# Kernel optimization log

Measured on AMD Instinct MI355X. Metric: run time of the kernel, lower is better.

## Reference

```python
import jax, jax.numpy as jnp
import numpy as np
from jax.scipy.special import gammaln

B, N, K = 16, 65536, 64


def setup_inputs() -> dict:
    key = jax.random.key(0)
    k1, k2, k3, k4, k5 = jax.random.split(key, 5)
    x = jax.random.normal(k1, (B, N), dtype=jnp.float32)
    loc = jnp.full((1,), 0.5, dtype=jnp.float32)          # mean of Normal alpha prior
    scale = jnp.full((1,), -2.0, dtype=jnp.float32)       # softplus(-2) ~ 0.127
    epsilon = jax.random.normal(k3, (1,), dtype=jnp.float32)
    lags = jax.random.randint(k4, (K,), 1, N - 1, dtype=jnp.int64)
    return {"x": x, "loc": loc, "scale": scale, "epsilon": epsilon, "lags": lags}


def _stochastic_frac_deriv(x, alpha, lags):
    """Monte-Carlo Marchaud fractional derivative with k sampled memory lags.

    D^a f(t) ~ a/Gamma(1-a) * (N-1)/k * sum_m (f(t) - f(t - j_m)) * j_m^{-a-1}
    with the term masked out when t < j_m (history does not exist).
    """
    n = x.shape[-1]
    k = lags.shape[0]
    j = jnp.clip(lags, 1, n - 1)                      # [k]
    t = jnp.arange(n)                                 # [N]
    idx = jnp.maximum(t[None, :] - j[:, None], 0)     # [k, N]
    mask = (t[None, :] >= j[:, None]).astype(x.dtype) # [k, N]
    w = j.astype(x.dtype) ** (-(alpha + 1.0))         # kernel weight s^{-a-1}, [k]
    c = alpha * jnp.exp(-gammaln(1.0 - alpha)) * (n - 1) / k  # normalization * MC volume
    xg = x[:, idx]                                    # [B, k, N] gathered history
    contrib = (x[:, None, :] - xg) * (mask * w[:, None])[None, :, :]
    return c * contrib.sum(axis=1)                    # [B, N]


def reference(x, loc, scale, epsilon, lags):
    # reparameterized alpha ~ Normal(loc, softplus(scale))
    alpha = (loc + jax.nn.softplus(scale) * epsilon)[0]
    alpha = jnp.clip(alpha, 0.01, 0.99)               # keep fractional order valid
    return _stochastic_frac_deriv(x, alpha, lags)
```

## Files before the change

kernel.cpp:

```cpp
#include <hip/hip_runtime.h>

#define BB 16
#define NN 65536
#define KK 64
#define TPB 256
#define CHUNK 512
#define NBLK ((BB * NN) / CHUNK)

__device__ __forceinline__ float readlane_f(float v, int lane) {
    return __uint_as_float((unsigned)__builtin_amdgcn_readlane((int)__float_as_uint(v), lane));
}

__global__ __launch_bounds__(TPB, 4) void frac_deriv_kernel(
    const float* __restrict__ x,
    const float* __restrict__ loc,
    const float* __restrict__ scale,
    const float* __restrict__ eps,
    const int* __restrict__ lags,
    float* __restrict__ out)
{
    __shared__ int   js_raw[KK];
    __shared__ float ws_raw[KK];
    __shared__ int   js[KK];
    __shared__ float ws[KK];

    const int tid  = threadIdx.x;
    const int lane = tid & 63;

    const int bid = blockIdx.x;
    const int swz = (bid & 7) * (NBLK / 8) + (bid >> 3);
    const int b   = swz >> 7;
    const int q   = 127 - (swz & 127);
    const int T   = q * CHUNK;

    const float* __restrict__ xr = x + (size_t)b * NN;
    const float xt0 = xr[T + tid];
    const float xt1 = xr[T + 256 + tid];

    if (tid < KK) {
        double s  = (double)scale[0];
        double sp = (s > 20.0) ? s : log1p(exp(s));
        double a  = (double)loc[0] + sp * (double)eps[0];
        a = fmin(fmax(a, 0.01), 0.99);
        double c = a * exp(-lgamma(1.0 - a)) * ((double)(NN - 1) / (double)KK);
        int j = lags[tid];
        j = (j < 1) ? 1 : ((j > NN - 1) ? NN - 1 : j);
        js_raw[tid] = j;
        ws_raw[tid] = (float)(c * exp(-(a + 1.0) * log((double)j)));
    }
    __syncthreads();
    if (tid < KK) {
        const int j = js_raw[tid];
        int rank = 0;
        for (int k = 0; k < KK; ++k) {
            const int jk = js_raw[k];
            rank += (int)((jk < j) || (jk == j && k < tid));
        }
        js[rank] = j;
        ws[rank] = ws_raw[tid];
    }
    __syncthreads();

    const int   jv = js[lane];
    const float wv = ws[lane];
    const int cf = __popcll(__ballot(jv <= T));
    const int cp = __popcll(__ballot(jv <= T + (CHUNK - 1)));
    const int cf16 = cf & ~15;

    double acc0 = 0.0, acc1 = 0.0;

    for (int mo = 0; mo < cf16; mo += 16) {
        float v0[16], v1[16];
#pragma unroll
        for (int mi = 0; mi < 16; ++mi) {
            const int jj = __builtin_amdgcn_readlane(jv, mo + mi);
            const float* bp = xr + (T - jj);
            v0[mi] = bp[tid];
            v1[mi] = bp[tid + 256];
        }
        float g0 = 0.0f, g1 = 0.0f;
#pragma unroll
        for (int mi = 0; mi < 16; ++mi) {
            const float wm = readlane_f(wv, mo + mi);
            g0 = fmaf(xt0 - v0[mi], wm, g0);
            g1 = fmaf(xt1 - v1[mi], wm, g1);
        }
        acc0 += (double)g0;
        acc1 += (double)g1;
    }

    for (int m = cf16; m < cp; ++m) {
        const int   jj = __builtin_amdgcn_readlane(jv, m);
        const float wm = readlane_f(wv, m);
        const int d0 = T + tid - jj;
        const int d1 = d0 + 256;
        const float g0v = xr[(d0 < 0) ? 0 : d0];
        const float g1v = xr[(d1 < 0) ? 0 : d1];
        acc0 += (d0 >= 0) ? (double)((xt0 - g0v) * wm) : 0.0;
        acc1 += (d1 >= 0) ? (double)((xt1 - g1v) * wm) : 0.0;
    }

    float* __restrict__ orow = out + (size_t)b * NN;
    orow[T + tid]       = (float)acc0;
    orow[T + 256 + tid] = (float)acc1;
}

extern "C" void kernel_launch(void* const* d_in, const int* in_sizes, int n_in,
                              void* d_out, int out_size, void* d_ws, size_t ws_size,
                              hipStream_t stream) {
    const float* x     = (const float*)d_in[0];
    const float* loc   = (const float*)d_in[1];
    const float* scale = (const float*)d_in[2];
    const float* eps   = (const float*)d_in[3];
    const int*   lags  = (const int*)d_in[4];
    float* out = (float*)d_out;

    frac_deriv_kernel<<<NBLK, TPB, 0, stream>>>(x, loc, scale, eps, lags, out);
}
```

Baseline: 18.14 us.

## Stage sorted-lag history windows in shared memory ring buffer with larger blocks

Each block now covers 2048 outputs with 1024 threads. Lags are grouped into spans that fit a 16K-float LDS ring buffer, and each span's history range is loaded cooperatively with float4 copies, skipping parts already loaded. The gathered reads then come from LDS instead of global/L2. The aim is to cut redundant global loads across lags, at the cost of many block barriers, lower occupancy from 64KB LDS and 1024-thread blocks, and fewer blocks (512).

```diff
diff --git a/kernel.cpp b/kernel.cpp
--- a/kernel.cpp
+++ b/kernel.cpp
@@ -3,15 +3,16 @@
 #define BB 16
 #define NN 65536
 #define KK 64
-#define TPB 256
-#define CHUNK 512
-#define NBLK ((BB * NN) / CHUNK)
+#define TPB 1024
+#define E   2048
+#define NBLK ((BB * NN) / E)
+#define W   16384
 
 __device__ __forceinline__ float readlane_f(float v, int lane) {
     return __uint_as_float((unsigned)__builtin_amdgcn_readlane((int)__float_as_uint(v), lane));
 }
 
-__global__ __launch_bounds__(TPB, 4) void frac_deriv_kernel(
+__global__ __launch_bounds__(TPB) void frac_deriv_kernel(
     const float* __restrict__ x,
     const float* __restrict__ loc,
     const float* __restrict__ scale,
@@ -19,6 +20,7 @@
     const int* __restrict__ lags,
     float* __restrict__ out)
 {
+    __shared__ float win[W];
     __shared__ int   js_raw[KK];
     __shared__ float ws_raw[KK];
     __shared__ int   js[KK];
@@ -29,13 +31,13 @@
 
     const int bid = blockIdx.x;
     const int swz = (bid & 7) * (NBLK / 8) + (bid >> 3);
-    const int b   = swz >> 7;
-    const int q   = 127 - (swz & 127);
-    const int T   = q * CHUNK;
+    const int b   = swz >> 5;
+    const int q   = 31 - (swz & 31);
+    const int T   = q * E;
 
     const float* __restrict__ xr = x + (size_t)b * NN;
     const float xt0 = xr[T + tid];
-    const float xt1 = xr[T + 256 + tid];
+    const float xt1 = xr[T + TPB + tid];
 
     if (tid < KK) {
         double s  = (double)scale[0];
@@ -64,45 +66,74 @@
     const int   jv = js[lane];
     const float wv = ws[lane];
     const int cf = __popcll(__ballot(jv <= T));
-    const int cp = __popcll(__ballot(jv <= T + (CHUNK - 1)));
-    const int cf16 = cf & ~15;
+    const int cp = __popcll(__ballot(jv <= T + (E - 1)));
 
     double acc0 = 0.0, acc1 = 0.0;
 
-    for (int mo = 0; mo < cf16; mo += 16) {
-        float v0[16], v1[16];
-#pragma unroll
-        for (int mi = 0; mi < 16; ++mi) {
-            const int jj = __builtin_amdgcn_readlane(jv, mo + mi);
-            const float* bp = xr + (T - jj);
-            v0[mi] = bp[tid];
-            v1[mi] = bp[tid + 256];
+    int m_hi = cf - 1;
+    int hi   = -(1 << 30);
+    while (m_hi >= 0) {
+        const int J0 = __builtin_amdgcn_readlane(jv, m_hi);
+        const int s0 = T - J0;
+        int m_lo = m_hi;
+        while (m_lo > 0) {
+            const int Jn = __builtin_amdgcn_readlane(jv, m_lo - 1);
+            if (J0 - Jn + E > W - 8) break;
+            --m_lo;
         }
-        float g0 = 0.0f, g1 = 0.0f;
-#pragma unroll
-        for (int mi = 0; mi < 16; ++mi) {
-            const float wm = readlane_f(wv, mo + mi);
-            g0 = fmaf(xt0 - v0[mi], wm, g0);
-            g1 = fmaf(xt1 - v1[mi], wm, g1);
+        const int J1      = __builtin_amdgcn_readlane(jv, m_lo);
+        const int need_hi = T - J1 + E;
+        const int a       = (s0 > hi) ? s0 : hi;
+
+        __syncthreads();
+        {
+            const int a4 = (a + 3) & ~3;
+            const int b4 = need_hi & ~3;
+            if (tid < a4 - a && a + tid < need_hi)
+                win[(a + tid) & (W - 1)] = xr[a + tid];
+            for (int i = a4 + 4 * tid; i + 4 <= need_hi; i += 4 * TPB) {
+                float4 v;
+                __builtin_memcpy(&v, xr + i, 16);
+                *(float4*)&win[i & (W - 1)] = v;
+            }
+            if (b4 >= a4 && tid < need_hi - b4)
+                win[(b4 + tid) & (W - 1)] = xr[b4 + tid];
+        }
+        hi = need_hi;
+        __syncthreads();
+
+        float g0 = 0.f, g1 = 0.f;
+        int cnt = 0;
+        for (int m = m_hi; m >= m_lo; --m) {
+            const int   jj = __builtin_amdgcn_readlane(jv, m);
+            const float wm = readlane_f(wv, m);
+            const int base = T + tid - jj;
+            g0 = fmaf(xt0 - win[ base        & (W - 1)], wm, g0);
+            g1 = fmaf(xt1 - win[(base + TPB) & (W - 1)], wm, g1);
+            if (++cnt == 8) {
+                acc0 += (double)g0; acc1 += (double)g1;
+                g0 = g1 = 0.f; cnt = 0;
+            }
         }
         acc0 += (double)g0;
         acc1 += (double)g1;
+        m_hi = m_lo - 1;
     }
 
-    for (int m = cf16; m < cp; ++m) {
+    for (int m = cf; m < cp; ++m) {
         const int   jj = __builtin_amdgcn_readlane(jv, m);
         const float wm = readlane_f(wv, m);
         const int d0 = T + tid - jj;
-        const int d1 = d0 + 256;
-        const float g0v = xr[(d0 < 0) ? 0 : d0];
-        const float g1v = xr[(d1 < 0) ? 0 : d1];
-        acc0 += (d0 >= 0) ? (double)((xt0 - g0v) * wm) : 0.0;
-        acc1 += (d1 >= 0) ? (double)((xt1 - g1v) * wm) : 0.0;
+        const int d1 = d0 + TPB;
+        const float p0 = xr[(d0 < 0) ? 0 : d0];
+        const float p1 = xr[(d1 < 0) ? 0 : d1];
+        acc0 += (d0 >= 0) ? (double)((xt0 - p0) * wm) : 0.0;
+        acc1 += (d1 >= 0) ? (double)((xt1 - p1) * wm) : 0.0;
     }
 
     float* __restrict__ orow = out + (size_t)b * NN;
     orow[T + tid]       = (float)acc0;
-    orow[T + 256 + tid] = (float)acc1;
+    orow[T + TPB + tid] = (float)acc1;
 }
 
 extern "C" void kernel_launch(void* const* d_in, const int* in_sizes, int n_in,
```

New measurement: 39.53 us. 118% more time.

## Balance work by pairing mirrored segments per block with float2 loads and barriers

Applied to the files above, without the earlier changes.

Replaces 2048 small 512-element blocks with 256 blocks of 1024 threads. Each block handles two mirrored 2048-element segments, an early one and a late one, so the number of active lags per block is roughly even. Loads and stores become float2-vectorised, the lag loop is unrolled by 4 instead of 16, and an s_barrier per iteration keeps the waves in lockstep to improve cache reuse of the shifted windows. The risks are lower occupancy with only 256 large blocks, and the barriers plus reduced unrolling may cut memory-level parallelism.

```diff
diff --git a/kernel.cpp b/kernel.cpp
--- a/kernel.cpp
+++ b/kernel.cpp
@@ -3,15 +3,22 @@
 #define BB 16
 #define NN 65536
 #define KK 64
-#define TPB 256
-#define CHUNK 512
-#define NBLK ((BB * NN) / CHUNK)
+#define TPB 1024
+#define ESEG 2048
+#define NPAIR 16
+#define NBLK (BB * NPAIR)
 
 __device__ __forceinline__ float readlane_f(float v, int lane) {
     return __uint_as_float((unsigned)__builtin_amdgcn_readlane((int)__float_as_uint(v), lane));
 }
 
-__global__ __launch_bounds__(TPB, 4) void frac_deriv_kernel(
+__device__ __forceinline__ float2 load2(const float* p) {
+    float2 v;
+    __builtin_memcpy(&v, p, 8);
+    return v;
+}
+
+__global__ __launch_bounds__(TPB) void frac_deriv_kernel(
     const float* __restrict__ x,
     const float* __restrict__ loc,
     const float* __restrict__ scale,
@@ -29,13 +36,16 @@
 
     const int bid = blockIdx.x;
     const int swz = (bid & 7) * (NBLK / 8) + (bid >> 3);
-    const int b   = swz >> 7;
-    const int q   = 127 - (swz & 127);
-    const int T   = q * CHUNK;
+    const int b   = swz >> 4;
+    const int p   = swz & 15;
+    const int TA  = p * ESEG;
+    const int TB  = (31 - p) * ESEG;
 
     const float* __restrict__ xr = x + (size_t)b * NN;
-    const float xt0 = xr[T + tid];
-    const float xt1 = xr[T + 256 + tid];
+    const int eA = TA + 2 * tid;
+    const int eB = TB + 2 * tid;
+    const float2 xtA = load2(xr + eA);
+    const float2 xtB = load2(xr + eB);
 
     if (tid < KK) {
         double s  = (double)scale[0];
@@ -63,46 +73,70 @@
 
     const int   jv = js[lane];
     const float wv = ws[lane];
-    const int cf = __popcll(__ballot(jv <= T));
-    const int cp = __popcll(__ballot(jv <= T + (CHUNK - 1)));
-    const int cf16 = cf & ~15;
+    const int cfA = __popcll(__ballot(jv <= TA));
+    const int cpA = __popcll(__ballot(jv <= TA + (ESEG - 1)));
+    const int cfB = __popcll(__ballot(jv <= TB));
+    const int cpB = __popcll(__ballot(jv <= TB + (ESEG - 1)));
 
-    double acc0 = 0.0, acc1 = 0.0;
+    double aA0 = 0.0, aA1 = 0.0, aB0 = 0.0, aB1 = 0.0;
 
-    for (int mo = 0; mo < cf16; mo += 16) {
-        float v0[16], v1[16];
-#pragma unroll
-        for (int mi = 0; mi < 16; ++mi) {
-            const int jj = __builtin_amdgcn_readlane(jv, mo + mi);
-            const float* bp = xr + (T - jj);
-            v0[mi] = bp[tid];
-            v1[mi] = bp[tid + 256];
-        }
-        float g0 = 0.0f, g1 = 0.0f;
-#pragma unroll
-        for (int mi = 0; mi < 16; ++mi) {
-            const float wm = readlane_f(wv, mo + mi);
-            g0 = fmaf(xt0 - v0[mi], wm, g0);
-            g1 = fmaf(xt1 - v1[mi], wm, g1);
-        }
-        acc0 += (double)g0;
-        acc1 += (double)g1;
+#define SEGLOOP(CF, E, XT, A0, A1)                                            \
+    {                                                                         \
+        const int cf4 = (CF) & ~3;                                            \
+        for (int mo = 0; mo < cf4; mo += 4) {                                 \
+            float2 u[4];                                                      \
+            _Pragma("unroll")                                                 \
+            for (int mi = 0; mi < 4; ++mi) {                                  \
+                const int jj = __builtin_amdgcn_readlane(jv, mo + mi);        \
+                u[mi] = load2(xr + ((E) - jj));                               \
+            }                                                                 \
+            float g0 = 0.f, g1 = 0.f;                                         \
+            _Pragma("unroll")                                                 \
+            for (int mi = 0; mi < 4; ++mi) {                                  \
+                const float wm = readlane_f(wv, mo + mi);                     \
+                g0 = fmaf((XT).x - u[mi].x, wm, g0);                          \
+                g1 = fmaf((XT).y - u[mi].y, wm, g1);                          \
+            }                                                                 \
+            A0 += (double)g0;                                                 \
+            A1 += (double)g1;                                                 \
+            __builtin_amdgcn_s_barrier();   \
+        }                                                                     \
+        for (int m = cf4; m < (CF); ++m) {                                    \
+            const int   jj = __builtin_amdgcn_readlane(jv, m);                \
+            const float wm = readlane_f(wv, m);                               \
+            const float2 u = load2(xr + ((E) - jj));                          \
+            A0 += (double)(((XT).x - u.x) * wm);                              \
+            A1 += (double)(((XT).y - u.y) * wm);                              \
+        }                                                                     \
     }
 
-    for (int m = cf16; m < cp; ++m) {
+    SEGLOOP(cfA, eA, xtA, aA0, aA1)
+    SEGLOOP(cfB, eB, xtB, aB0, aB1)
+
+    for (int m = cfA; m < cpA; ++m) {
         const int   jj = __builtin_amdgcn_readlane(jv, m);
         const float wm = readlane_f(wv, m);
-        const int d0 = T + tid - jj;
-        const int d1 = d0 + 256;
-        const float g0v = xr[(d0 < 0) ? 0 : d0];
-        const float g1v = xr[(d1 < 0) ? 0 : d1];
-        acc0 += (d0 >= 0) ? (double)((xt0 - g0v) * wm) : 0.0;
-        acc1 += (d1 >= 0) ? (double)((xt1 - g1v) * wm) : 0.0;
+        const int d0 = eA - jj, d1 = d0 + 1;
+        const float u0 = xr[(d0 < 0) ? 0 : d0];
+        const float u1 = xr[(d1 < 0) ? 0 : d1];
+        aA0 += (d0 >= 0) ? (double)((xtA.x - u0) * wm) : 0.0;
+        aA1 += (d1 >= 0) ? (double)((xtA.y - u1) * wm) : 0.0;
+    }
+    for (int m = cfB; m < cpB; ++m) {
+        const int   jj = __builtin_amdgcn_readlane(jv, m);
+        const float wm = readlane_f(wv, m);
+        const int d0 = eB - jj, d1 = d0 + 1;
+        const float u0 = xr[(d0 < 0) ? 0 : d0];
+        const float u1 = xr[(d1 < 0) ? 0 : d1];
+        aB0 += (d0 >= 0) ? (double)((xtB.x - u0) * wm) : 0.0;
+        aB1 += (d1 >= 0) ? (double)((xtB.y - u1) * wm) : 0.0;
     }
 
     float* __restrict__ orow = out + (size_t)b * NN;
-    orow[T + tid]       = (float)acc0;
-    orow[T + 256 + tid] = (float)acc1;
+    float2 rA = make_float2((float)aA0, (float)aA1);
+    float2 rB = make_float2((float)aB0, (float)aB1);
+    __builtin_memcpy(orow + eA, &rA, 8);
+    __builtin_memcpy(orow + eB, &rB, 8);
 }
 
 extern "C" void kernel_launch(void* const* d_in, const int* in_sizes, int n_in,
```

Result: slower. 19.29 us (+6.3%).
